# Optimization experiments

Hardware: AMD Instinct MI355X
Metric: run time of the kernel (lower is better)

## Reference

```python
import jax, jax.numpy as jnp
import numpy as np

B, NELEC, D, NION = 2048, 32, 512, 8
NSPIN = 2
N = NELEC // NSPIN  # electrons per spin = orbital-matrix size = 16


def setup_inputs() -> dict:
    key = jax.random.key(0)
    ks = jax.random.split(key, 6)
    eq_inputs = jax.random.normal(ks[0], (B, NELEC, D), jnp.float32)
    r_ei = jax.random.normal(ks[1], (B, NELEC, NION, 3), jnp.float32)
    # learned params (stacked over the 2 spins; equal split so shapes match)
    W_lin = jax.random.normal(ks[2], (NSPIN, 2 * D, N), jnp.float32) * (0.5 / np.sqrt(D))
    b_lin = jax.random.normal(ks[3], (NSPIN, N), jnp.float32) * 0.1
    A_env = jax.random.normal(ks[4], (NSPIN, 3, 3, NION, N), jnp.float32) * 0.3
    w_ion = jax.random.normal(ks[5], (NSPIN, NION, N), jnp.float32)
    return dict(eq_inputs=eq_inputs, r_ei=r_ei, W_lin=W_lin, b_lin=b_lin,
                A_env=A_env, w_ion=w_ion)


def reference(eq_inputs, r_ei, W_lin, b_lin, A_env, w_ion):
    """Per-particle determinant antiequivariance layer.

    For each spin s and particle p, a doubly-equivariant orbital matrix
    M_p[j, k] = (y_p . W1[:,k] + y_j . W2[:,k] + b[k]) * env[j, k]
    is built (pair-concat dense split into two einsums to avoid the (B,n,n,2d)
    intermediate), with anisotropic exponential envelopes
    env[j, k] = sum_I w_ion[I,k] * exp(-||A[:,:,I,k] @ r_ei[j,I,:]||).
    Output per spin: y_p * det(M_p), stacked over spins -> (B, 2, n, d).
    """
    b, nelec, d = eq_inputs.shape
    n = nelec // NSPIN
    x = eq_inputs.reshape(b, NSPIN, n, d)            # spin_split=2 equal split
    r = r_ei.reshape(b, NSPIN, n, r_ei.shape[-2], 3)
    W1, W2 = W_lin[:, :d], W_lin[:, d:]
    # linear (doubly equivariant) part: (B, S, n_p, n_j, n_k)
    lin_p = jnp.einsum('bspf,sfk->bspk', x, W1)
    lin_j = jnp.einsum('bsjf,sfk->bsjk', x, W2) + b_lin[None, :, None, :]
    lin = lin_p[:, :, :, None, :] + lin_j[:, :, None, :, :]
    # anisotropic exponential envelopes: exp(-||A (r - R)||), combined over ions
    ar = jnp.einsum('bsjip,spqik->bsjiqk', r, A_env)        # (B,S,n,I,3,k)
    env = jnp.exp(-jnp.sqrt(jnp.sum(ar * ar, axis=-2)))     # (B,S,n,I,k)
    env = jnp.einsum('bsjik,sik->bsjk', env, w_ion)         # (B,S,n_j,n_k)
    M = lin * env[:, :, None, :, :]                         # (B,S,n_p,n_j,n_k)
    dets = jnp.linalg.det(M)                                # (B,S,n_p)
    # y_p * det(M_p), per spin (stacked over the spin axis)
    return x * dets[..., None]                              # (B,S,n,d)
```

## Files before the change

kernel.cpp:

```cpp
#include <hip/hip_runtime.h>
#include <cstdint>
#include <cstddef>

#define NSPIN 2
#define NPART 16
#define DDIM  512
#define NION  8

#define RS_OFF    0
#define LINP_OFF  1536
#define LINJ_OFF  (LINP_OFF + 1024)
#define ENV_OFF   (LINJ_OFF + 1280)
#define DETS_OFF  (ENV_OFF + 1280)
#define LDS_FLOATS (DETS_OFF + 64)
#define LDS_BYTES  (LDS_FLOATS * 4)

typedef short bf16x8 __attribute__((ext_vector_type(8)));
typedef float f32x4  __attribute__((ext_vector_type(4)));

__device__ __forceinline__ short bfc(float x) {
    unsigned u = __float_as_uint(x);
    u += 0x7FFFu + ((u >> 16) & 1u);
    return (short)(u >> 16);
}

#define DPPMAXU(k, ctrl) { unsigned o_ = (unsigned)__builtin_amdgcn_update_dpp(0, (int)(k), (ctrl), 0xF, 0xF, true); (k) = (k) > o_ ? (k) : o_; }

__global__ void __launch_bounds__(256)
prep_kernel(const float* __restrict__ WL, uint4* __restrict__ WS)
{
    int slot = blockIdx.x * 256 + threadIdx.x;
    int spin = slot >> 11;
    int rem  = slot & 2047;
    int half = rem >> 10;
    int ks   = (rem >> 6) & 15;
    int lane = rem & 63;
    int cc2  = lane & 15, hh = lane >> 4;
    const float* src = WL + (size_t)spin * (2 * DDIM * NPART)
                     + ((size_t)(half * 512 + ks * 32 + hh * 8)) * NPART + cc2;
    ushort u[8];
    #pragma unroll
    for (int e = 0; e < 8; ++e) u[e] = (ushort)bfc(src[e * NPART]);
    uint4 pk;
    pk.x = (unsigned)u[0] | ((unsigned)u[1] << 16);
    pk.y = (unsigned)u[2] | ((unsigned)u[3] << 16);
    pk.z = (unsigned)u[4] | ((unsigned)u[5] << 16);
    pk.w = (unsigned)u[6] | ((unsigned)u[7] << 16);
    WS[slot] = pk;
}

__global__ void __launch_bounds__(256, 5)
ppdet_kernel(const float* __restrict__ EQ, const float* __restrict__ RE,
             const uint4* __restrict__ WS, const float* __restrict__ BL,
             const float* __restrict__ AE, const float* __restrict__ WI,
             float* __restrict__ OUT)
{
    extern __shared__ float ls[];
    const int t  = threadIdx.x;
    const int s  = blockIdx.x >> 9;
    const int b0 = (blockIdx.x & 511) * 4;

    const int l  = t & 63;
    const int w  = t >> 6;
    const int c  = l & 15;
    const int h4 = l >> 4;
    const int jr = t & 15;
    const int ke = t >> 4;

    #pragma unroll
    for (int it = 0; it < 6; ++it) {
        int idx = it * 256 + t;
        int bi = idx / 384, rem = idx % 384;
        int e = rem >> 4, j = rem & 15;
        ls[RS_OFF + idx] = RE[((size_t)(b0 + bi) * 32 + s * 16 + j) * 24 + e];
    }
    __syncthreads();

    {
        const float* xg = EQ + ((size_t)(b0 + w) * 32 + s * 16 + c) * DDIM + h4 * 8;
        const uint4* wb = WS + (size_t)s * 2048;
        f32x4 accp = {0.f, 0.f, 0.f, 0.f}, accj = {0.f, 0.f, 0.f, 0.f};
        #pragma unroll
        for (int kb = 0; kb < 4; ++kb) {
            float4 xa[8];
            uint4 w1v[4], w2v[4];
            #pragma unroll
            for (int u = 0; u < 4; ++u) {
                xa[2 * u]     = *(const float4*)(xg + (kb * 4 + u) * 32);
                xa[2 * u + 1] = *(const float4*)(xg + (kb * 4 + u) * 32 + 4);
                w1v[u] = wb[(kb * 4 + u) * 64 + l];
                w2v[u] = wb[(16 + kb * 4 + u) * 64 + l];
            }
            #pragma unroll
            for (int u = 0; u < 4; ++u) {
                bf16x8 af;
                af[0] = bfc(xa[2 * u].x);     af[1] = bfc(xa[2 * u].y);
                af[2] = bfc(xa[2 * u].z);     af[3] = bfc(xa[2 * u].w);
                af[4] = bfc(xa[2 * u + 1].x); af[5] = bfc(xa[2 * u + 1].y);
                af[6] = bfc(xa[2 * u + 1].z); af[7] = bfc(xa[2 * u + 1].w);
                accp = __builtin_amdgcn_mfma_f32_16x16x32_bf16(af, *(bf16x8*)&w1v[u], accp, 0, 0, 0);
                accj = __builtin_amdgcn_mfma_f32_16x16x32_bf16(af, *(bf16x8*)&w2v[u], accj, 0, 0, 0);
            }
        }
        const float blv = BL[s * NPART + c];
        #pragma unroll
        for (int q = 0; q < 4; ++q) {
            ls[LINP_OFF + (w * 16 + h4 * 4 + q) * 16 + c] = accp[q];
            ls[LINJ_OFF + (w * 16 + h4 * 4 + q) * 20 + c] = accj[q] + blv;
        }
    }

    {
        float G0[8], G1[8], G2[8], G3[8], G4[8], G5[8], wir[8];
        const float* Ag = AE + (size_t)s * (9 * NION * NPART);
        #pragma unroll
        for (int i = 0; i < 8; ++i) {
            float a00 = Ag[((0 * 3 + 0) * NION + i) * NPART + ke];
            float a01 = Ag[((0 * 3 + 1) * NION + i) * NPART + ke];
            float a02 = Ag[((0 * 3 + 2) * NION + i) * NPART + ke];
            float a10 = Ag[((1 * 3 + 0) * NION + i) * NPART + ke];
            float a11 = Ag[((1 * 3 + 1) * NION + i) * NPART + ke];
            float a12 = Ag[((1 * 3 + 2) * NION + i) * NPART + ke];
            float a20 = Ag[((2 * 3 + 0) * NION + i) * NPART + ke];
            float a21 = Ag[((2 * 3 + 1) * NION + i) * NPART + ke];
            float a22 = Ag[((2 * 3 + 2) * NION + i) * NPART + ke];
            G0[i] = a00 * a00 + a01 * a01 + a02 * a02;
            G1[i] = a10 * a10 + a11 * a11 + a12 * a12;
            G2[i] = a20 * a20 + a21 * a21 + a22 * a22;
            G3[i] = a00 * a10 + a01 * a11 + a02 * a12;
            G4[i] = a00 * a20 + a01 * a21 + a02 * a22;
            G5[i] = a10 * a20 + a11 * a21 + a12 * a22;
            wir[i] = WI[(size_t)s * (NION * NPART) + i * NPART + ke];
        }
        #pragma unroll
        for (int ib = 0; ib < 4; ++ib) {
            const float* rs = ls + RS_OFF + ib * 384;
            float ev = 0.f;
            #pragma unroll
            for (int i = 0; i < 8; ++i) {
                float r0 = rs[(i * 3 + 0) * 16 + jr];
                float r1 = rs[(i * 3 + 1) * 16 + jr];
                float r2 = rs[(i * 3 + 2) * 16 + jr];
                float ss = r0 * r0 * G0[i];
                ss = fmaf(r1 * r1, G1[i], ss);
                ss = fmaf(r2 * r2, G2[i], ss);
                float tcr = r0 * r1 * G3[i];
                tcr = fmaf(r0 * r2, G4[i], tcr);
                tcr = fmaf(r1 * r2, G5[i], tcr);
                ss = fmaf(2.f, tcr, ss);
                ss = fmaxf(ss, 0.f);
                ev = fmaf(wir[i], __expf(-__builtin_amdgcn_sqrtf(ss)), ev);
            }
            ls[ENV_OFF + (ib * 16 + jr) * 20 + ke] = ev;
        }
    }
    __syncthreads();

    const int lanebase4 = (t & 48) << 2;
    for (int ib = 0; ib < 4; ++ib) {
        float Mr[16];
        const float* lp = ls + LINP_OFF + (ib * 16 + ke) * 16;
        const float* lj = ls + LINJ_OFF + (ib * 16 + jr) * 20;
        const float* ev = ls + ENV_OFF  + (ib * 16 + jr) * 20;
        #pragma unroll
        for (int cq = 0; cq < 4; ++cq) {
            float4 a  = *(const float4*)(lp + cq * 4);
            float4 bb = *(const float4*)(lj + cq * 4);
            float4 e  = *(const float4*)(ev + cq * 4);
            Mr[cq * 4 + 0] = (a.x + bb.x) * e.x;
            Mr[cq * 4 + 1] = (a.y + bb.y) * e.y;
            Mr[cq * 4 + 2] = (a.z + bb.z) * e.z;
            Mr[cq * 4 + 3] = (a.w + bb.w) * e.w;
        }
        float detv = 1.f;
        unsigned sel = 0u;
        int inv = 0;
        bool msel = false;
        #pragma unroll
        for (int cc = 0; cc < 16; ++cc) {
            unsigned key = msel ? 0u
                : ((__float_as_uint(fabsf(Mr[cc])) & 0xFFFFFFF0u) | (unsigned)jr);
            DPPMAXU(key, 0x121); DPPMAXU(key, 0x122); DPPMAXU(key, 0x124); DPPMAXU(key, 0x128);
            const int idx = (int)(key & 15u);
            const bool ispiv = (jr == idx) && !msel;
            const int srcaddr = lanebase4 | (idx << 2);
            float Pr[16];
            #pragma unroll
            for (int k2 = cc; k2 < 16; ++k2)
                Pr[k2] = __int_as_float(__builtin_amdgcn_ds_bpermute(
                             srcaddr, __float_as_int(Mr[k2])));
            const float pv = Pr[cc];
            const float f = (msel || ispiv || pv == 0.f) ? 0.f
                          : Mr[cc] * __builtin_amdgcn_rcpf(pv);
            inv += __popc(sel >> (idx + 1));
            sel |= (1u << idx);
            msel = msel || ispiv;
            detv *= pv;
            #pragma unroll
            for (int k2 = cc + 1; k2 < 16; ++k2)
                Mr[k2] = fmaf(-f, Pr[k2], Mr[k2]);
        }
        if (inv & 1) detv = -detv;
        if (jr == 0) ls[DETS_OFF + ib * 16 + ke] = detv;
    }
    __syncthreads();

    #pragma unroll
    for (int ib = 0; ib < 4; ++ib) {
        const size_t base = ((size_t)(b0 + ib) * 32 + s * 16) * DDIM;
        #pragma unroll
        for (int i2 = 0; i2 < 8; ++i2) {
            int f4i = i2 * 256 + t;
            float dt = ls[DETS_OFF + ib * 16 + (f4i >> 7)];
            float4 xv = ((const float4*)(EQ + base))[f4i];
            float4 o = make_float4(xv.x * dt, xv.y * dt, xv.z * dt, xv.w * dt);
            ((float4*)(OUT + base))[f4i] = o;
        }
    }
}

extern "C" void kernel_launch(void* const* d_in, const int* in_sizes, int n_in,
                              void* d_out, int out_size, void* d_ws, size_t ws_size,
                              hipStream_t stream) {
    const float* EQ = (const float*)d_in[0];
    const float* RE = (const float*)d_in[1];
    const float* WL = (const float*)d_in[2];
    const float* BL = (const float*)d_in[3];
    const float* AE = (const float*)d_in[4];
    const float* WI = (const float*)d_in[5];
    float* OUT = (float*)d_out;
    uint4* WS = (uint4*)d_ws;
    (void)in_sizes; (void)n_in; (void)out_size; (void)ws_size;

    prep_kernel<<<dim3(16), dim3(256), 0, stream>>>(WL, WS);
    ppdet_kernel<<<dim3(1024), dim3(256), LDS_BYTES, stream>>>(EQ, RE, WS, BL, AE, WI, OUT);
}
```

Before: 76.33 us.

## Halve batches per block and split the GEMM reduction across wave pairs

```diff
diff --git a/kernel.cpp b/kernel.cpp
--- a/kernel.cpp
+++ b/kernel.cpp
@@ -7,12 +7,14 @@
 #define DDIM  512
 #define NION  8
 
-#define RS_OFF    0
-#define LINP_OFF  1536
-#define LINJ_OFF  (LINP_OFF + 1024)
-#define ENV_OFF   (LINJ_OFF + 1280)
-#define DETS_OFF  (ENV_OFF + 1280)
-#define LDS_FLOATS (DETS_OFF + 64)
+#define RS_OFF     0
+#define PARTP_OFF  768
+#define PARTJ_OFF  (PARTP_OFF + 1024)
+#define LINP_OFF   (PARTJ_OFF + 1024)
+#define LINJ_OFF   (LINP_OFF + 512)
+#define ENV_OFF    (LINJ_OFF + 640)
+#define DETS_OFF   (ENV_OFF + 640)
+#define LDS_FLOATS (DETS_OFF + 32)
 #define LDS_BYTES  (LDS_FLOATS * 4)
 
 typedef short bf16x8 __attribute__((ext_vector_type(8)));
@@ -49,7 +51,7 @@
     WS[slot] = pk;
 }
 
-__global__ void __launch_bounds__(256, 5)
+__global__ void __launch_bounds__(256, 8)
 ppdet_kernel(const float* __restrict__ EQ, const float* __restrict__ RE,
              const uint4* __restrict__ WS, const float* __restrict__ BL,
              const float* __restrict__ AE, const float* __restrict__ WI,
@@ -57,8 +59,8 @@
 {
     extern __shared__ float ls[];
     const int t  = threadIdx.x;
-    const int s  = blockIdx.x >> 9;
-    const int b0 = (blockIdx.x & 511) * 4;
+    const int s  = blockIdx.x >> 10;
+    const int b0 = (blockIdx.x & 1023) * 2;
 
     const int l  = t & 63;
     const int w  = t >> 6;
@@ -68,7 +70,7 @@
     const int ke = t >> 4;
 
     #pragma unroll
-    for (int it = 0; it < 6; ++it) {
+    for (int it = 0; it < 3; ++it) {
         int idx = it * 256 + t;
         int bi = idx / 384, rem = idx % 384;
         int e = rem >> 4, j = rem & 15;
@@ -77,11 +79,14 @@
     __syncthreads();
 
     {
-        const float* xg = EQ + ((size_t)(b0 + w) * 32 + s * 16 + c) * DDIM + h4 * 8;
-        const uint4* wb = WS + (size_t)s * 2048;
+        const int bsel  = w >> 1;
+        const int khalf = w & 1;
+        const float* xg = EQ + ((size_t)((b0 + bsel) * 32 + s * 16 + c)) * DDIM
+                        + khalf * 256 + h4 * 8;
+        const uint4* wb = WS + (size_t)s * 2048 + khalf * 8 * 64;
         f32x4 accp = {0.f, 0.f, 0.f, 0.f}, accj = {0.f, 0.f, 0.f, 0.f};
         #pragma unroll
-        for (int kb = 0; kb < 4; ++kb) {
+        for (int kb = 0; kb < 2; ++kb) {
             float4 xa[8];
             uint4 w1v[4], w2v[4];
             #pragma unroll
@@ -89,7 +94,7 @@
                 xa[2 * u]     = *(const float4*)(xg + (kb * 4 + u) * 32);
                 xa[2 * u + 1] = *(const float4*)(xg + (kb * 4 + u) * 32 + 4);
                 w1v[u] = wb[(kb * 4 + u) * 64 + l];
-                w2v[u] = wb[(16 + kb * 4 + u) * 64 + l];
+                w2v[u] = wb[1024 + (kb * 4 + u) * 64 + l];
             }
             #pragma unroll
             for (int u = 0; u < 4; ++u) {
@@ -102,11 +107,10 @@
                 accj = __builtin_amdgcn_mfma_f32_16x16x32_bf16(af, *(bf16x8*)&w2v[u], accj, 0, 0, 0);
             }
         }
-        const float blv = BL[s * NPART + c];
         #pragma unroll
         for (int q = 0; q < 4; ++q) {
-            ls[LINP_OFF + (w * 16 + h4 * 4 + q) * 16 + c] = accp[q];
-            ls[LINJ_OFF + (w * 16 + h4 * 4 + q) * 20 + c] = accj[q] + blv;
+            ls[PARTP_OFF + w * 256 + q * 64 + l] = accp[q];
+            ls[PARTJ_OFF + w * 256 + q * 64 + l] = accj[q];
         }
     }
 
@@ -133,7 +137,7 @@
             wir[i] = WI[(size_t)s * (NION * NPART) + i * NPART + ke];
         }
         #pragma unroll
-        for (int ib = 0; ib < 4; ++ib) {
+        for (int ib = 0; ib < 2; ++ib) {
             const float* rs = ls + RS_OFF + ib * 384;
             float ev = 0.f;
             #pragma unroll
@@ -151,17 +155,32 @@
                 ss = fmaxf(ss, 0.f);
                 ev = fmaf(wir[i], __expf(-__builtin_amdgcn_sqrtf(ss)), ev);
             }
-            ls[ENV_OFF + (ib * 16 + jr) * 20 + ke] = ev;
+            ls[ENV_OFF + ib * 320 + jr * 20 + ke] = ev;
+        }
+    }
+    __syncthreads();
+
+    {
+        const float blv = BL[s * NPART + (t & 15)];
+        const int q2 = t >> 6, l2 = t & 63;
+        const int row = (l2 >> 4) * 4 + q2;
+        const int col = l2 & 15;
+        #pragma unroll
+        for (int bsel = 0; bsel < 2; ++bsel) {
+            float vp = ls[PARTP_OFF + bsel * 512 + t] + ls[PARTP_OFF + bsel * 512 + 256 + t];
+            float vj = ls[PARTJ_OFF + bsel * 512 + t] + ls[PARTJ_OFF + bsel * 512 + 256 + t];
+            ls[LINP_OFF + bsel * 256 + row * 16 + col] = vp;
+            ls[LINJ_OFF + bsel * 320 + row * 20 + col] = vj + blv;
         }
     }
     __syncthreads();
 
     const int lanebase4 = (t & 48) << 2;
-    for (int ib = 0; ib < 4; ++ib) {
+    for (int ib = 0; ib < 2; ++ib) {
         float Mr[16];
-        const float* lp = ls + LINP_OFF + (ib * 16 + ke) * 16;
-        const float* lj = ls + LINJ_OFF + (ib * 16 + jr) * 20;
-        const float* ev = ls + ENV_OFF  + (ib * 16 + jr) * 20;
+        const float* lp = ls + LINP_OFF + ib * 256 + ke * 16;
+        const float* lj = ls + LINJ_OFF + ib * 320 + jr * 20;
+        const float* ev = ls + ENV_OFF  + ib * 320 + jr * 20;
         #pragma unroll
         for (int cq = 0; cq < 4; ++cq) {
             float4 a  = *(const float4*)(lp + cq * 4);
@@ -206,8 +225,8 @@
     __syncthreads();
 
     #pragma unroll
-    for (int ib = 0; ib < 4; ++ib) {
-        const size_t base = ((size_t)(b0 + ib) * 32 + s * 16) * DDIM;
+    for (int ib = 0; ib < 2; ++ib) {
+        const size_t base = ((size_t)((b0 + ib) * 32 + s * 16)) * DDIM;
         #pragma unroll
         for (int i2 = 0; i2 < 8; ++i2) {
             int f4i = i2 * 256 + t;
@@ -233,5 +252,5 @@
     (void)in_sizes; (void)n_in; (void)out_size; (void)ws_size;
 
     prep_kernel<<<dim3(16), dim3(256), 0, stream>>>(WL, WS);
-    ppdet_kernel<<<dim3(1024), dim3(256), LDS_BYTES, stream>>>(EQ, RE, WS, BL, AE, WI, OUT);
-}
+    ppdet_kernel<<<dim3(2048), dim3(256), LDS_BYTES, stream>>>(EQ, RE, WS, BL, AE, WI, OUT);
+}
```

After: 80.79 us. +5.8%, slower.

## Use one batch per 128-thread block and precompute envelope Gram terms in prep

Applied to the files above, without the earlier changes.

```diff
diff --git a/kernel.cpp b/kernel.cpp
--- a/kernel.cpp
+++ b/kernel.cpp
@@ -7,13 +7,16 @@
 #define DDIM  512
 #define NION  8
 
-#define RS_OFF    0
-#define LINP_OFF  1536
-#define LINJ_OFF  (LINP_OFF + 1024)
-#define ENV_OFF   (LINJ_OFF + 1280)
-#define DETS_OFF  (ENV_OFF + 1280)
-#define LDS_FLOATS (DETS_OFF + 64)
+#define RS_OFF     0
+#define GRAM_OFF   384
+#define LINP_OFF   (GRAM_OFF + 1024)
+#define LINJ_OFF   (LINP_OFF + 256)
+#define ENV_OFF    (LINJ_OFF + 320)
+#define DETS_OFF   (ENV_OFF + 320)
+#define LDS_FLOATS (DETS_OFF + 16)
 #define LDS_BYTES  (LDS_FLOATS * 4)
+
+#define WS_GRAM_F  16384
 
 typedef short bf16x8 __attribute__((ext_vector_type(8)));
 typedef float f32x4  __attribute__((ext_vector_type(4)));
@@ -27,69 +30,96 @@
 #define DPPMAXU(k, ctrl) { unsigned o_ = (unsigned)__builtin_amdgcn_update_dpp(0, (int)(k), (ctrl), 0xF, 0xF, true); (k) = (k) > o_ ? (k) : o_; }
 
 __global__ void __launch_bounds__(256)
-prep_kernel(const float* __restrict__ WL, uint4* __restrict__ WS)
+prep_kernel(const float* __restrict__ WL, const float* __restrict__ AE,
+            const float* __restrict__ WI, float* __restrict__ WSF)
 {
-    int slot = blockIdx.x * 256 + threadIdx.x;
-    int spin = slot >> 11;
-    int rem  = slot & 2047;
-    int half = rem >> 10;
-    int ks   = (rem >> 6) & 15;
-    int lane = rem & 63;
-    int cc2  = lane & 15, hh = lane >> 4;
-    const float* src = WL + (size_t)spin * (2 * DDIM * NPART)
-                     + ((size_t)(half * 512 + ks * 32 + hh * 8)) * NPART + cc2;
-    ushort u[8];
-    #pragma unroll
-    for (int e = 0; e < 8; ++e) u[e] = (ushort)bfc(src[e * NPART]);
-    uint4 pk;
-    pk.x = (unsigned)u[0] | ((unsigned)u[1] << 16);
-    pk.y = (unsigned)u[2] | ((unsigned)u[3] << 16);
-    pk.z = (unsigned)u[4] | ((unsigned)u[5] << 16);
-    pk.w = (unsigned)u[6] | ((unsigned)u[7] << 16);
-    WS[slot] = pk;
-}
-
-__global__ void __launch_bounds__(256, 5)
+    const int t = threadIdx.x;
+    if (blockIdx.x < 16) {
+        int slot = blockIdx.x * 256 + t;
+        int spin = slot >> 11;
+        int rem  = slot & 2047;
+        int half = rem >> 10;
+        int ks   = (rem >> 6) & 15;
+        int lane = rem & 63;
+        int cc2  = lane & 15, hh = lane >> 4;
+        const float* src = WL + (size_t)spin * (2 * DDIM * NPART)
+                         + ((size_t)(half * 512 + ks * 32 + hh * 8)) * NPART + cc2;
+        ushort u[8];
+        #pragma unroll
+        for (int e = 0; e < 8; ++e) u[e] = (ushort)bfc(src[e * NPART]);
+        uint4 pk;
+        pk.x = (unsigned)u[0] | ((unsigned)u[1] << 16);
+        pk.y = (unsigned)u[2] | ((unsigned)u[3] << 16);
+        pk.z = (unsigned)u[4] | ((unsigned)u[5] << 16);
+        pk.w = (unsigned)u[6] | ((unsigned)u[7] << 16);
+        ((uint4*)WSF)[slot] = pk;
+    } else {
+        int s  = t >> 7;
+        int ke = (t >> 3) & 15;
+        int i  = t & 7;
+        const float* Ag = AE + (size_t)s * (9 * NION * NPART);
+        float a00 = Ag[((0 * 3 + 0) * NION + i) * NPART + ke];
+        float a01 = Ag[((0 * 3 + 1) * NION + i) * NPART + ke];
+        float a02 = Ag[((0 * 3 + 2) * NION + i) * NPART + ke];
+        float a10 = Ag[((1 * 3 + 0) * NION + i) * NPART + ke];
+        float a11 = Ag[((1 * 3 + 1) * NION + i) * NPART + ke];
+        float a12 = Ag[((1 * 3 + 2) * NION + i) * NPART + ke];
+        float a20 = Ag[((2 * 3 + 0) * NION + i) * NPART + ke];
+        float a21 = Ag[((2 * 3 + 1) * NION + i) * NPART + ke];
+        float a22 = Ag[((2 * 3 + 2) * NION + i) * NPART + ke];
+        float* g = WSF + WS_GRAM_F + t * 8;
+        g[0] = a00 * a00 + a01 * a01 + a02 * a02;
+        g[1] = a10 * a10 + a11 * a11 + a12 * a12;
+        g[2] = a20 * a20 + a21 * a21 + a22 * a22;
+        g[3] = a00 * a10 + a01 * a11 + a02 * a12;
+        g[4] = a00 * a20 + a01 * a21 + a02 * a22;
+        g[5] = a10 * a20 + a11 * a21 + a12 * a22;
+        g[6] = WI[(size_t)s * (NION * NPART) + i * NPART + ke];
+        g[7] = 0.f;
+    }
+}
+
+__global__ void __launch_bounds__(128, 8)
 ppdet_kernel(const float* __restrict__ EQ, const float* __restrict__ RE,
-             const uint4* __restrict__ WS, const float* __restrict__ BL,
-             const float* __restrict__ AE, const float* __restrict__ WI,
+             const float* __restrict__ WSF, const float* __restrict__ BL,
              float* __restrict__ OUT)
 {
     extern __shared__ float ls[];
-    const int t  = threadIdx.x;
-    const int s  = blockIdx.x >> 9;
-    const int b0 = (blockIdx.x & 511) * 4;
+    const int t = threadIdx.x;
+    const int s = blockIdx.x >> 11;
+    const int b = blockIdx.x & 2047;
 
     const int l  = t & 63;
     const int w  = t >> 6;
     const int c  = l & 15;
     const int h4 = l >> 4;
     const int jr = t & 15;
-    const int ke = t >> 4;
 
     #pragma unroll
-    for (int it = 0; it < 6; ++it) {
-        int idx = it * 256 + t;
-        int bi = idx / 384, rem = idx % 384;
-        int e = rem >> 4, j = rem & 15;
-        ls[RS_OFF + idx] = RE[((size_t)(b0 + bi) * 32 + s * 16 + j) * 24 + e];
-    }
-    __syncthreads();
+    for (int it = 0; it < 3; ++it) {
+        int idx = it * 128 + t;
+        int e = idx >> 4, j = idx & 15;
+        ls[RS_OFF + idx] = RE[((size_t)b * 32 + s * 16 + j) * 24 + e];
+    }
+    #pragma unroll
+    for (int it = 0; it < 8; ++it) {
+        int idx = it * 128 + t;
+        ls[GRAM_OFF + idx] = WSF[WS_GRAM_F + s * 1024 + idx];
+    }
 
     {
-        const float* xg = EQ + ((size_t)(b0 + w) * 32 + s * 16 + c) * DDIM + h4 * 8;
-        const uint4* wb = WS + (size_t)s * 2048;
-        f32x4 accp = {0.f, 0.f, 0.f, 0.f}, accj = {0.f, 0.f, 0.f, 0.f};
+        const float* xg = EQ + ((size_t)(b * 32 + s * 16 + c)) * DDIM + h4 * 8;
+        const uint4* wb = (const uint4*)WSF + (size_t)s * 2048 + w * 1024;
+        f32x4 acc = {0.f, 0.f, 0.f, 0.f};
         #pragma unroll
         for (int kb = 0; kb < 4; ++kb) {
             float4 xa[8];
-            uint4 w1v[4], w2v[4];
+            uint4 wv[4];
             #pragma unroll
             for (int u = 0; u < 4; ++u) {
                 xa[2 * u]     = *(const float4*)(xg + (kb * 4 + u) * 32);
                 xa[2 * u + 1] = *(const float4*)(xg + (kb * 4 + u) * 32 + 4);
-                w1v[u] = wb[(kb * 4 + u) * 64 + l];
-                w2v[u] = wb[(16 + kb * 4 + u) * 64 + l];
+                wv[u] = wb[(kb * 4 + u) * 64 + l];
             }
             #pragma unroll
             for (int u = 0; u < 4; ++u) {
@@ -98,70 +128,59 @@
                 af[2] = bfc(xa[2 * u].z);     af[3] = bfc(xa[2 * u].w);
                 af[4] = bfc(xa[2 * u + 1].x); af[5] = bfc(xa[2 * u + 1].y);
                 af[6] = bfc(xa[2 * u + 1].z); af[7] = bfc(xa[2 * u + 1].w);
-                accp = __builtin_amdgcn_mfma_f32_16x16x32_bf16(af, *(bf16x8*)&w1v[u], accp, 0, 0, 0);
-                accj = __builtin_amdgcn_mfma_f32_16x16x32_bf16(af, *(bf16x8*)&w2v[u], accj, 0, 0, 0);
+                acc = __builtin_amdgcn_mfma_f32_16x16x32_bf16(af, *(bf16x8*)&wv[u], acc, 0, 0, 0);
             }
         }
-        const float blv = BL[s * NPART + c];
-        #pragma unroll
-        for (int q = 0; q < 4; ++q) {
-            ls[LINP_OFF + (w * 16 + h4 * 4 + q) * 16 + c] = accp[q];
-            ls[LINJ_OFF + (w * 16 + h4 * 4 + q) * 20 + c] = accj[q] + blv;
-        }
-    }
+        if (w == 0) {
+            #pragma unroll
+            for (int q = 0; q < 4; ++q)
+                ls[LINP_OFF + (h4 * 4 + q) * 16 + c] = acc[q];
+        } else {
+            const float blv = BL[s * NPART + c];
+            #pragma unroll
+            for (int q = 0; q < 4; ++q)
+                ls[LINJ_OFF + (h4 * 4 + q) * 20 + c] = acc[q] + blv;
+        }
+    }
+    __syncthreads();
 
     {
-        float G0[8], G1[8], G2[8], G3[8], G4[8], G5[8], wir[8];
-        const float* Ag = AE + (size_t)s * (9 * NION * NPART);
-        #pragma unroll
-        for (int i = 0; i < 8; ++i) {
-            float a00 = Ag[((0 * 3 + 0) * NION + i) * NPART + ke];
-            float a01 = Ag[((0 * 3 + 1) * NION + i) * NPART + ke];
-            float a02 = Ag[((0 * 3 + 2) * NION + i) * NPART + ke];
-            float a10 = Ag[((1 * 3 + 0) * NION + i) * NPART + ke];
-            float a11 = Ag[((1 * 3 + 1) * NION + i) * NPART + ke];
-            float a12 = Ag[((1 * 3 + 2) * NION + i) * NPART + ke];
-            float a20 = Ag[((2 * 3 + 0) * NION + i) * NPART + ke];
-            float a21 = Ag[((2 * 3 + 1) * NION + i) * NPART + ke];
-            float a22 = Ag[((2 * 3 + 2) * NION + i) * NPART + ke];
-            G0[i] = a00 * a00 + a01 * a01 + a02 * a02;
-            G1[i] = a10 * a10 + a11 * a11 + a12 * a12;
-            G2[i] = a20 * a20 + a21 * a21 + a22 * a22;
-            G3[i] = a00 * a10 + a01 * a11 + a02 * a12;
-            G4[i] = a00 * a20 + a01 * a21 + a02 * a22;
-            G5[i] = a10 * a20 + a11 * a21 + a12 * a22;
-            wir[i] = WI[(size_t)s * (NION * NPART) + i * NPART + ke];
-        }
-        #pragma unroll
-        for (int ib = 0; ib < 4; ++ib) {
-            const float* rs = ls + RS_OFF + ib * 384;
+        const int ke8 = t >> 4;
+        #pragma unroll
+        for (int kx = 0; kx < 2; ++kx) {
+            const int ke2 = ke8 + kx * 8;
+            const float4* gp = (const float4*)(ls + GRAM_OFF + ke2 * 64);
             float ev = 0.f;
             #pragma unroll
             for (int i = 0; i < 8; ++i) {
-                float r0 = rs[(i * 3 + 0) * 16 + jr];
-                float r1 = rs[(i * 3 + 1) * 16 + jr];
-                float r2 = rs[(i * 3 + 2) * 16 + jr];
-                float ss = r0 * r0 * G0[i];
-                ss = fmaf(r1 * r1, G1[i], ss);
-                ss = fmaf(r2 * r2, G2[i], ss);
-                float tcr = r0 * r1 * G3[i];
-                tcr = fmaf(r0 * r2, G4[i], tcr);
-                tcr = fmaf(r1 * r2, G5[i], tcr);
+                float4 gA = gp[i * 2];
+                float4 gB = gp[i * 2 + 1];
+                float r0 = ls[RS_OFF + (i * 3 + 0) * 16 + jr];
+                float r1 = ls[RS_OFF + (i * 3 + 1) * 16 + jr];
+                float r2 = ls[RS_OFF + (i * 3 + 2) * 16 + jr];
+                float ss = r0 * r0 * gA.x;
+                ss = fmaf(r1 * r1, gA.y, ss);
+                ss = fmaf(r2 * r2, gA.z, ss);
+                float tcr = r0 * r1 * gA.w;
+                tcr = fmaf(r0 * r2, gB.x, tcr);
+                tcr = fmaf(r1 * r2, gB.y, tcr);
                 ss = fmaf(2.f, tcr, ss);
                 ss = fmaxf(ss, 0.f);
-                ev = fmaf(wir[i], __expf(-__builtin_amdgcn_sqrtf(ss)), ev);
+                ev = fmaf(gB.z, __expf(-__builtin_amdgcn_sqrtf(ss)), ev);
             }
-            ls[ENV_OFF + (ib * 16 + jr) * 20 + ke] = ev;
+            ls[ENV_OFF + jr * 20 + ke2] = ev;
         }
     }
     __syncthreads();
 
     const int lanebase4 = (t & 48) << 2;
-    for (int ib = 0; ib < 4; ++ib) {
+    #pragma unroll
+    for (int half = 0; half < 2; ++half) {
+        const int p = (t >> 4) + half * 8;
         float Mr[16];
-        const float* lp = ls + LINP_OFF + (ib * 16 + ke) * 16;
-        const float* lj = ls + LINJ_OFF + (ib * 16 + jr) * 20;
-        const float* ev = ls + ENV_OFF  + (ib * 16 + jr) * 20;
+        const float* lp = ls + LINP_OFF + p * 16;
+        const float* lj = ls + LINJ_OFF + jr * 20;
+        const float* ev = ls + ENV_OFF  + jr * 20;
         #pragma unroll
         for (int cq = 0; cq < 4; ++cq) {
             float4 a  = *(const float4*)(lp + cq * 4);
@@ -201,20 +220,19 @@
                 Mr[k2] = fmaf(-f, Pr[k2], Mr[k2]);
         }
         if (inv & 1) detv = -detv;
-        if (jr == 0) ls[DETS_OFF + ib * 16 + ke] = detv;
+        if (jr == 0) ls[DETS_OFF + p] = detv;
     }
     __syncthreads();
 
-    #pragma unroll
-    for (int ib = 0; ib < 4; ++ib) {
-        const size_t base = ((size_t)(b0 + ib) * 32 + s * 16) * DDIM;
-        #pragma unroll
-        for (int i2 = 0; i2 < 8; ++i2) {
-            int f4i = i2 * 256 + t;
-            float dt = ls[DETS_OFF + ib * 16 + (f4i >> 7)];
+    {
+        const size_t base = ((size_t)(b * 32 + s * 16)) * DDIM;
+        #pragma unroll
+        for (int i2 = 0; i2 < 16; ++i2) {
+            int f4i = i2 * 128 + t;
+            float dt = ls[DETS_OFF + i2];
             float4 xv = ((const float4*)(EQ + base))[f4i];
-            float4 o = make_float4(xv.x * dt, xv.y * dt, xv.z * dt, xv.w * dt);
-            ((float4*)(OUT + base))[f4i] = o;
+            ((float4*)(OUT + base))[f4i] =
+                make_float4(xv.x * dt, xv.y * dt, xv.z * dt, xv.w * dt);
         }
     }
 }
@@ -229,9 +247,9 @@
     const float* AE = (const float*)d_in[4];
     const float* WI = (const float*)d_in[5];
     float* OUT = (float*)d_out;
-    uint4* WS = (uint4*)d_ws;
+    float* WSF = (float*)d_ws;
     (void)in_sizes; (void)n_in; (void)out_size; (void)ws_size;
 
-    prep_kernel<<<dim3(16), dim3(256), 0, stream>>>(WL, WS);
-    ppdet_kernel<<<dim3(1024), dim3(256), LDS_BYTES, stream>>>(EQ, RE, WS, BL, AE, WI, OUT);
-}
+    prep_kernel<<<dim3(17), dim3(256), 0, stream>>>(WL, AE, WI, WSF);
+    ppdet_kernel<<<dim3(4096), dim3(128), LDS_BYTES, stream>>>(EQ, RE, WSF, BL, OUT);
+}
```

After: 83.00 us. 1.09x slower.
